# Kernel tuning notes

Hardware: AMD Instinct MI355X
Metric: run time of the kernel (lower is better)

The kernel has to match this reference:

```python
import jax, jax.numpy as jnp
import numpy as np

L = 3        # num_hidden_layers
H = 512      # hidden_features
DIN = 4      # in_features
D = DIN - 1  # u-branch input dim
N = 65536    # batch of query points


def setup_inputs() -> dict:
    key = jax.random.key(0)
    ks = jax.random.split(key, 16)

    def w(k, shape, fan_in):
        # kaiming-normal-ish init (relu), matches init_weights_normal in spirit
        return jax.random.normal(k, shape, jnp.float32) * (2.0 / fan_in) ** 0.5

    return {
        "coords": jax.random.normal(ks[0], (N, DIN), jnp.float32),
        # net_u: (D->H), then (H->H) x (L-1)
        "Wu0": w(ks[1], (D, H), D), "bu0": jnp.zeros((H,), jnp.float32),
        "Wu": w(ks[2], (L - 1, H, H), H), "bu": jnp.zeros((L - 1, H), jnp.float32),
        # net_zu_u: (H->H) x L
        "Wzuu": w(ks[3], (L, H, H), H), "bzuu": jnp.zeros((L, H), jnp.float32),
        # net_z_zu: (H->H) x (L-1), last (H->1), no bias
        "Wzzu": w(ks[4], (L - 1, H, H), H), "Wzzu_last": w(ks[5], (H, 1), H),
        # net_yu_u: (D->1), then (H->1) x L
        "Wyuu0": w(ks[6], (D, 1), D), "byuu0": jnp.zeros((1,), jnp.float32),
        "Wyuu": w(ks[7], (L, H, 1), H), "byuu": jnp.zeros((L, 1), jnp.float32),
        # net_z_yu: (1->H) x L, last (1->1), no bias
        "Wzyu": w(ks[8], (L, 1, H), 1), "Wzyu_last": w(ks[9], (1, 1), 1),
        # net_z_u: (D->H), (H->H) x (L-1), last (H->1)
        "Wzu0": w(ks[10], (D, H), D), "bzu0": jnp.zeros((H,), jnp.float32),
        "Wzu": w(ks[11], (L - 1, H, H), H), "bzu": jnp.zeros((L - 1, H), jnp.float32),
        "Wzu_last": w(ks[12], (H, 1), H), "bzu_last": jnp.zeros((1,), jnp.float32),
        # learned scalar scales
        "p": jnp.float32(0.1), "pu": jnp.float32(0.1), "pzu": jnp.float32(0.1),
    }


def reference(coords, Wu0, bu0, Wu, bu, Wzuu, bzuu, Wzzu, Wzzu_last,
              Wyuu0, byuu0, Wyuu, byuu, Wzyu, Wzyu_last,
              Wzu0, bzu0, Wzu, bzu, Wzu_last, bzu_last, p, pu, pzu):
    relu = jax.nn.relu  # nonlinearity='relu' -> nl == nl_u == relu; dropout inactive (eval)
    y = coords[..., -1:]   # [N, 1]
    u = coords[..., :-1]   # [N, D]
    # layer 0
    z = (u @ Wzu0 + bzu0) + (y * (u @ Wyuu0 + byuu0)) @ Wzyu[0]  # [N, H]
    z = relu(10.0 * p * z)
    u = relu(10.0 * pu * (u @ Wu0 + bu0))  # [N, H]
    for i in range(1, L + 1):
        zz = z * relu(10.0 * pzu * (u @ Wzuu[i - 1] + bzuu[i - 1]))
        t1 = zz @ (Wzzu[i - 1] if i < L else Wzzu_last)
        t2 = (u @ Wzu[i - 1] + bzu[i - 1]) if i < L else (u @ Wzu_last + bzu_last)
        yy = y * (u @ Wyuu[i - 1] + byuu[i - 1])  # [N, 1]
        t3 = yy @ (Wzyu[i] if i < L else Wzyu_last)
        z = t1 + t2 + t3
        if i == L:
            return z  # [N, 1]
        z_out = relu(10.0 * p * z)
        u = relu(10.0 * pu * (u @ Wu[i - 1] + bu[i - 1]))
        z = z_out
    return z
```

## Files before the change

### kernel.cpp

```cpp
#include <hip/hip_runtime.h>
#include <stdint.h>
#include <stddef.h>


typedef float  f32x4 __attribute__((ext_vector_type(4)));
typedef __bf16 bf16x8 __attribute__((ext_vector_type(8)));

__device__ __forceinline__ int act_idx(int row, int k){
  return ((k>>5)<<11) | ((row>>4)<<9) | (((k>>3)&3)<<7) | ((row&15)<<3) | (k&7);
}

__global__ void prep_weights(const float* __restrict__ Wzuu, const float* __restrict__ Wzzu,
                             const float* __restrict__ Wzu,  const float* __restrict__ Wu,
                             __bf16* __restrict__ Wb)
{
  int gid = blockIdx.x * 256 + threadIdx.x;
  int m   = gid >> 16;
  int rem = gid & 65535;
  int k   = rem >> 7;
  int j0  = (rem & 127) << 2;
  const float* src;
  if      (m < 3) src = Wzuu + (size_t)m     * 262144;
  else if (m < 5) src = Wzzu + (size_t)(m-3) * 262144;
  else if (m < 7) src = Wzu  + (size_t)(m-5) * 262144;
  else            src = Wu   + (size_t)(m-7) * 262144;
  const float4 v = *(const float4*)(src + k*512 + j0);
  const int base = m << 18;
  #pragma unroll
  for (int e = 0; e < 4; ++e){
    const int j = j0 + e;
    const float x = (e==0) ? v.x : (e==1) ? v.y : (e==2) ? v.z : v.w;
    const int off = ((k>>5)<<14) | ((j>>4)<<9)
                  | ((((j&15) | (((k>>3)&3)<<4)))<<3) | (k&7);
    Wb[base + off] = (__bf16)x;
  }
}

__device__ __forceinline__ void gemm_acc(const __bf16* __restrict__ a_lds,
                                         const __bf16* __restrict__ wb,
                                         f32x4 acc[4][4],
                                         int wv, int lane)
{
  const __bf16* wp = wb + ((wv<<2)<<9) + (lane<<3);
  bf16x8 a0[4], a1[4], b0[4], b1[4];
  #pragma unroll
  for (int jt = 0; jt < 4; ++jt)
    b0[jt] = *(const bf16x8*)(wp + (jt<<9));
  #pragma unroll
  for (int rt = 0; rt < 4; ++rt)
    a0[rt] = *(const bf16x8*)(a_lds + (rt<<9) + (lane<<3));
  #pragma unroll
  for (int kt = 0; kt < 16; kt += 2){
    #pragma unroll
    for (int jt = 0; jt < 4; ++jt)
      b1[jt] = *(const bf16x8*)(wp + ((kt+1)<<14) + (jt<<9));
    #pragma unroll
    for (int rt = 0; rt < 4; ++rt)
      a1[rt] = *(const bf16x8*)(a_lds + ((kt+1)<<11) + (rt<<9) + (lane<<3));
    #pragma unroll
    for (int jt = 0; jt < 4; ++jt)
      #pragma unroll
      for (int rt = 0; rt < 4; ++rt)
        acc[rt][jt] = __builtin_amdgcn_mfma_f32_16x16x32_bf16(a0[rt], b0[jt], acc[rt][jt], 0, 0, 0);
    if (kt + 2 < 16){
      #pragma unroll
      for (int jt = 0; jt < 4; ++jt)
        b0[jt] = *(const bf16x8*)(wp + ((kt+2)<<14) + (jt<<9));
      #pragma unroll
      for (int rt = 0; rt < 4; ++rt)
        a0[rt] = *(const bf16x8*)(a_lds + ((kt+2)<<11) + (rt<<9) + (lane<<3));
    }
    #pragma unroll
    for (int jt = 0; jt < 4; ++jt)
      #pragma unroll
      for (int rt = 0; rt < 4; ++rt)
        acc[rt][jt] = __builtin_amdgcn_mfma_f32_16x16x32_bf16(a1[rt], b1[jt], acc[rt][jt], 0, 0, 0);
  }
}

__global__ __launch_bounds__(512, 2) void fc_fused(
    const float* __restrict__ coords,
    const __bf16* __restrict__ Wb,
    const float* __restrict__ Wu0,  const float* __restrict__ bu0,
    const float* __restrict__ bu,
    const float* __restrict__ bzuu,
    const float* __restrict__ Wzzu_last,
    const float* __restrict__ Wyuu0, const float* __restrict__ byuu0,
    const float* __restrict__ Wyuu,  const float* __restrict__ byuu,
    const float* __restrict__ Wzyu,  const float* __restrict__ Wzyu_last,
    const float* __restrict__ Wzu0,  const float* __restrict__ bzu0,
    const float* __restrict__ bzu,
    const float* __restrict__ Wzu_last, const float* __restrict__ bzu_last,
    const float* __restrict__ p, const float* __restrict__ pu, const float* __restrict__ pzu,
    float* __restrict__ out)
{
  __shared__ __align__(16) __bf16 u_lds [32768];
  __shared__ __align__(16) __bf16 zz_lds[32768];

  const int tid  = threadIdx.x;
  const int lane = tid & 63;
  const int wv   = tid >> 6;
  const int n0   = blockIdx.x << 6;

  const float P  = 10.f * p[0];
  const float PU = 10.f * pu[0];
  const float PZ = 10.f * pzu[0];

  const float y_l = coords[(size_t)(n0 + lane)*4 + 3];

  for (int s = tid; s < 4096; s += 512){
    const int row = s >> 6;
    const int k0  = (s & 63) << 3;
    const float* c = coords + (size_t)(n0 + row)*4;
    const float c0 = c[0], c1 = c[1], c2 = c[2], yy = c[3];
    const float s0 = c0*Wyuu0[0] + c1*Wyuu0[1] + c2*Wyuu0[2] + byuu0[0];
    bf16x8 pu8, pz8;
    #pragma unroll
    for (int e = 0; e < 8; ++e){
      const int k = k0 + e;
      const float uv = c0*Wu0[k]  + c1*Wu0[512+k]  + c2*Wu0[1024+k]  + bu0[k];
      pu8[e] = (__bf16)fmaxf(PU*uv, 0.f);
      const float zv = c0*Wzu0[k] + c1*Wzu0[512+k] + c2*Wzu0[1024+k] + bzu0[k]
                     + yy*s0*Wzyu[k];
      pz8[e] = (__bf16)fmaxf(P*zv, 0.f);
    }
    *(bf16x8*)(u_lds  + act_idx(row, k0)) = pu8;
    *(bf16x8*)(zz_lds + act_idx(row, k0)) = pz8;
  }
  __syncthreads();

  f32x4 acc[4][4];

  for (int it = 0; it < 3; ++it){
    float s_val = byuu[it];
    {
      const float* wc = Wyuu + it*512;
      for (int kb = 0; kb < 64; ++kb){
        bf16x8 v = *(const bf16x8*)(u_lds + act_idx(lane, kb<<3));
        #pragma unroll
        for (int e = 0; e < 8; ++e) s_val += (float)v[e] * wc[(kb<<3)+e];
      }
    }

    #pragma unroll
    for (int rt = 0; rt < 4; ++rt)
      #pragma unroll
      for (int jt = 0; jt < 4; ++jt)
        acc[rt][jt] = (f32x4){0.f,0.f,0.f,0.f};
    gemm_acc(u_lds, Wb + ((size_t)it<<18), acc, wv, lane);
    #pragma unroll
    for (int jt = 0; jt < 4; ++jt){
      const int col = (wv<<6) + (jt<<4) + (lane & 15);
      const float bz = bzuu[it*512 + col];
      #pragma unroll
      for (int rt = 0; rt < 4; ++rt){
        #pragma unroll
        for (int rr = 0; rr < 4; ++rr){
          const int row = (rt<<4) + ((lane>>4)<<2) + rr;
          const int idx = act_idx(row, col);
          const float zold = (float)zz_lds[idx];
          const float t    = acc[rt][jt][rr] + bz;
          zz_lds[idx] = (__bf16)(zold * fmaxf(PZ*t, 0.f));
        }
      }
    }
    __syncthreads();

    if (it < 2){
      #pragma unroll
      for (int rt = 0; rt < 4; ++rt)
        #pragma unroll
        for (int jt = 0; jt < 4; ++jt)
          acc[rt][jt] = (f32x4){0.f,0.f,0.f,0.f};
      gemm_acc(zz_lds, Wb + ((size_t)(3+it)<<18), acc, wv, lane);
      gemm_acc(u_lds,  Wb + ((size_t)(5+it)<<18), acc, wv, lane);
      __syncthreads();

      float yvv[4][4], svv[4][4];
      #pragma unroll
      for (int rt = 0; rt < 4; ++rt)
        #pragma unroll
        for (int rr = 0; rr < 4; ++rr){
          const int row = (rt<<4) + ((lane>>4)<<2) + rr;
          yvv[rt][rr] = __shfl(y_l,  row);
          svv[rt][rr] = __shfl(s_val, row);
        }
      #pragma unroll
      for (int jt = 0; jt < 4; ++jt){
        const int col = (wv<<6) + (jt<<4) + (lane & 15);
        const float bz  = bzu[it*512 + col];
        const float wzy = Wzyu[(it+1)*512 + col];
        #pragma unroll
        for (int rt = 0; rt < 4; ++rt){
          #pragma unroll
          for (int rr = 0; rr < 4; ++rr){
            const int row = (rt<<4) + ((lane>>4)<<2) + rr;
            const float zn = acc[rt][jt][rr] + bz + yvv[rt][rr]*svv[rt][rr]*wzy;
            zz_lds[act_idx(row, col)] = (__bf16)fmaxf(P*zn, 0.f);
          }
        }
      }

      #pragma unroll
      for (int rt = 0; rt < 4; ++rt)
        #pragma unroll
        for (int jt = 0; jt < 4; ++jt)
          acc[rt][jt] = (f32x4){0.f,0.f,0.f,0.f};
      gemm_acc(u_lds, Wb + ((size_t)(7+it)<<18), acc, wv, lane);
      __syncthreads();
      #pragma unroll
      for (int jt = 0; jt < 4; ++jt){
        const int col = (wv<<6) + (jt<<4) + (lane & 15);
        const float bb = bu[it*512 + col];
        #pragma unroll
        for (int rt = 0; rt < 4; ++rt){
          #pragma unroll
          for (int rr = 0; rr < 4; ++rr){
            const int row = (rt<<4) + ((lane>>4)<<2) + rr;
            u_lds[act_idx(row, col)] = (__bf16)fmaxf(PU*(acc[rt][jt][rr] + bb), 0.f);
          }
        }
      }
      __syncthreads();
    } else {
      const int row = tid >> 3;
      const int q   = tid & 7;
      float av = 0.f, au = 0.f;
      for (int kb = q*8; kb < q*8 + 8; ++kb){
        const int k0 = kb << 3;
        bf16x8 vz = *(const bf16x8*)(zz_lds + act_idx(row, k0));
        bf16x8 vu = *(const bf16x8*)(u_lds  + act_idx(row, k0));
        #pragma unroll
        for (int e = 0; e < 8; ++e){
          av += (float)vz[e] * Wzzu_last[k0+e];
          au += (float)vu[e] * Wzu_last [k0+e];
        }
      }
      float tot = av + au;
      tot += __shfl_xor(tot, 1);
      tot += __shfl_xor(tot, 2);
      tot += __shfl_xor(tot, 4);
      const float yv = __shfl(y_l,  row & 63);
      const float sv = __shfl(s_val, row & 63);
      if (q == 0)
        out[n0 + row] = tot + bzu_last[0] + yv*sv*Wzyu_last[0];
    }
  }
}

extern "C" void kernel_launch(void* const* d_in, const int* in_sizes, int n_in,
                              void* d_out, int out_size, void* d_ws, size_t ws_size,
                              hipStream_t stream)
{
  const float* coords    = (const float*)d_in[0];
  const float* Wu0       = (const float*)d_in[1];
  const float* bu0       = (const float*)d_in[2];
  const float* Wu        = (const float*)d_in[3];
  const float* bu        = (const float*)d_in[4];
  const float* Wzuu      = (const float*)d_in[5];
  const float* bzuu      = (const float*)d_in[6];
  const float* Wzzu      = (const float*)d_in[7];
  const float* Wzzu_last = (const float*)d_in[8];
  const float* Wyuu0     = (const float*)d_in[9];
  const float* byuu0     = (const float*)d_in[10];
  const float* Wyuu      = (const float*)d_in[11];
  const float* byuu      = (const float*)d_in[12];
  const float* Wzyu      = (const float*)d_in[13];
  const float* Wzyu_last = (const float*)d_in[14];
  const float* Wzu0      = (const float*)d_in[15];
  const float* bzu0      = (const float*)d_in[16];
  const float* Wzu       = (const float*)d_in[17];
  const float* bzu       = (const float*)d_in[18];
  const float* Wzu_last  = (const float*)d_in[19];
  const float* bzu_last  = (const float*)d_in[20];
  const float* p         = (const float*)d_in[21];
  const float* pu        = (const float*)d_in[22];
  const float* pzu       = (const float*)d_in[23];

  __bf16* Wb = (__bf16*)d_ws;

  prep_weights<<<2304, 256, 0, stream>>>(Wzuu, Wzzu, Wzu, Wu, Wb);

  fc_fused<<<1024, 512, 0, stream>>>(
      coords, Wb,
      Wu0, bu0, bu, bzuu, Wzzu_last,
      Wyuu0, byuu0, Wyuu, byuu, Wzyu, Wzyu_last,
      Wzu0, bzu0, bzu, Wzu_last, bzu_last,
      p, pu, pzu,
      (float*)d_out);
}
```

Baseline: 408.0 us.

## Prefetch next GEMM weights across calls and split the yu dot product across waves

The GEMM helper now keeps a three-deep ring of weight fragments and, in its last two k-steps, loads the first two weight fragments of the next GEMM in the chain. This is meant to hide global-load latency at GEMM boundaries and through each k-loop. The per-row Wyuu dot product was previously computed redundantly by every wave with 64 serial loads per lane. It is now split across the 8 waves, reduced with shuffles, and combined through a small shared-memory buffer. The extra live fragment registers raise register pressure under launch_bounds(512,2), which could cause spills.

```diff
diff --git a/kernel.cpp b/kernel.cpp
--- a/kernel.cpp
+++ b/kernel.cpp
@@ -38,43 +38,41 @@
 
 __device__ __forceinline__ void gemm_acc(const __bf16* __restrict__ a_lds,
                                          const __bf16* __restrict__ wb,
+                                         const __bf16* __restrict__ wb_next,
+                                         bf16x8 bpre[2][4],
                                          f32x4 acc[4][4],
                                          int wv, int lane)
 {
-  const __bf16* wp = wb + ((wv<<2)<<9) + (lane<<3);
-  bf16x8 a0[4], a1[4], b0[4], b1[4];
+  const int woff = ((wv<<2)<<9) + (lane<<3);
+  const __bf16* wp = wb + woff;
+  bf16x8 b[3][4];
+  bf16x8 a[2][4];
   #pragma unroll
-  for (int jt = 0; jt < 4; ++jt)
-    b0[jt] = *(const bf16x8*)(wp + (jt<<9));
+  for (int jt = 0; jt < 4; ++jt){ b[0][jt] = bpre[0][jt]; b[1][jt] = bpre[1][jt]; }
   #pragma unroll
   for (int rt = 0; rt < 4; ++rt)
-    a0[rt] = *(const bf16x8*)(a_lds + (rt<<9) + (lane<<3));
+    a[0][rt] = *(const bf16x8*)(a_lds + (rt<<9) + (lane<<3));
   #pragma unroll
-  for (int kt = 0; kt < 16; kt += 2){
+  for (int kt = 0; kt < 16; ++kt){
+    if (kt < 14){
+      #pragma unroll
+      for (int jt = 0; jt < 4; ++jt)
+        b[(kt+2)%3][jt] = *(const bf16x8*)(wp + ((kt+2)<<14) + (jt<<9));
+    } else {
+      #pragma unroll
+      for (int jt = 0; jt < 4; ++jt)
+        bpre[kt-14][jt] = *(const bf16x8*)(wb_next + woff + ((kt-14)<<14) + (jt<<9));
+    }
+    if (kt < 15){
+      #pragma unroll
+      for (int rt = 0; rt < 4; ++rt)
+        a[(kt+1)&1][rt] = *(const bf16x8*)(a_lds + ((kt+1)<<11) + (rt<<9) + (lane<<3));
+    }
     #pragma unroll
     for (int jt = 0; jt < 4; ++jt)
-      b1[jt] = *(const bf16x8*)(wp + ((kt+1)<<14) + (jt<<9));
-    #pragma unroll
-    for (int rt = 0; rt < 4; ++rt)
-      a1[rt] = *(const bf16x8*)(a_lds + ((kt+1)<<11) + (rt<<9) + (lane<<3));
-    #pragma unroll
-    for (int jt = 0; jt < 4; ++jt)
-      #pragma unroll
-      for (int rt = 0; rt < 4; ++rt)
-        acc[rt][jt] = __builtin_amdgcn_mfma_f32_16x16x32_bf16(a0[rt], b0[jt], acc[rt][jt], 0, 0, 0);
-    if (kt + 2 < 16){
-      #pragma unroll
-      for (int jt = 0; jt < 4; ++jt)
-        b0[jt] = *(const bf16x8*)(wp + ((kt+2)<<14) + (jt<<9));
-      #pragma unroll
-      for (int rt = 0; rt < 4; ++rt)
-        a0[rt] = *(const bf16x8*)(a_lds + ((kt+2)<<11) + (rt<<9) + (lane<<3));
-    }
-    #pragma unroll
-    for (int jt = 0; jt < 4; ++jt)
-      #pragma unroll
-      for (int rt = 0; rt < 4; ++rt)
-        acc[rt][jt] = __builtin_amdgcn_mfma_f32_16x16x32_bf16(a1[rt], b1[jt], acc[rt][jt], 0, 0, 0);
+      #pragma unroll
+      for (int rt = 0; rt < 4; ++rt)
+        acc[rt][jt] = __builtin_amdgcn_mfma_f32_16x16x32_bf16(a[kt&1][rt], b[kt%3][jt], acc[rt][jt], 0, 0, 0);
   }
 }
 
@@ -96,6 +94,7 @@
 {
   __shared__ __align__(16) __bf16 u_lds [32768];
   __shared__ __align__(16) __bf16 zz_lds[32768];
+  __shared__ float sp_lds[2][64];
 
   const int tid  = threadIdx.x;
   const int lane = tid & 63;
@@ -107,6 +106,16 @@
   const float PZ = 10.f * pzu[0];
 
   const float y_l = coords[(size_t)(n0 + lane)*4 + 3];
+
+  bf16x8 bpre[2][4];
+  {
+    const int woff = ((wv<<2)<<9) + (lane<<3);
+    #pragma unroll
+    for (int s2 = 0; s2 < 2; ++s2)
+      #pragma unroll
+      for (int jt = 0; jt < 4; ++jt)
+        bpre[s2][jt] = *(const bf16x8*)(Wb + woff + (s2<<14) + (jt<<9));
+  }
 
   for (int s = tid; s < 4096; s += 512){
     const int row = s >> 6;
@@ -132,14 +141,31 @@
   f32x4 acc[4][4];
 
   for (int it = 0; it < 3; ++it){
-    float s_val = byuu[it];
+    const __bf16* w_p1 = Wb + ((size_t)it     << 18);
+    const __bf16* w_zz = Wb + ((size_t)(3+it) << 18);
+    const __bf16* w_zu = Wb + ((size_t)(5+it) << 18);
+    const __bf16* w_u  = Wb + ((size_t)(7+it) << 18);
+    const __bf16* w_n1 = (it < 2) ? w_zz : w_p1;
+    const __bf16* w_nx = (it < 2) ? (Wb + ((size_t)(it+1) << 18)) : w_p1;
+
     {
-      const float* wc = Wyuu + it*512;
-      for (int kb = 0; kb < 64; ++kb){
-        bf16x8 v = *(const bf16x8*)(u_lds + act_idx(lane, kb<<3));
-        #pragma unroll
-        for (int e = 0; e < 8; ++e) s_val += (float)v[e] * wc[(kb<<3)+e];
-      }
+      const float* wc = Wyuu + (it<<9);
+      const int rt = wv & 3;
+      const int kh = wv >> 2;
+      float pp = 0.f;
+      #pragma unroll
+      for (int t = 0; t < 8; ++t){
+        const int kt = (kh<<3) + t;
+        const int k0 = (kt<<5) + ((lane>>4)<<3);
+        bf16x8 v = *(const bf16x8*)(u_lds + (kt<<11) + (rt<<9) + (lane<<3));
+        const float4 w0 = *(const float4*)(wc + k0);
+        const float4 w1 = *(const float4*)(wc + k0 + 4);
+        pp += (float)v[0]*w0.x + (float)v[1]*w0.y + (float)v[2]*w0.z + (float)v[3]*w0.w
+            + (float)v[4]*w1.x + (float)v[5]*w1.y + (float)v[6]*w1.z + (float)v[7]*w1.w;
+      }
+      pp += __shfl_xor(pp, 16);
+      pp += __shfl_xor(pp, 32);
+      if (lane < 16) sp_lds[kh][(rt<<4) + lane] = pp;
     }
 
     #pragma unroll
@@ -147,11 +173,11 @@
       #pragma unroll
       for (int jt = 0; jt < 4; ++jt)
         acc[rt][jt] = (f32x4){0.f,0.f,0.f,0.f};
-    gemm_acc(u_lds, Wb + ((size_t)it<<18), acc, wv, lane);
+    gemm_acc(u_lds, w_p1, w_n1, bpre, acc, wv, lane);
     #pragma unroll
     for (int jt = 0; jt < 4; ++jt){
       const int col = (wv<<6) + (jt<<4) + (lane & 15);
-      const float bz = bzuu[it*512 + col];
+      const float bz = bzuu[(it<<9) + col];
       #pragma unroll
       for (int rt = 0; rt < 4; ++rt){
         #pragma unroll
@@ -172,30 +198,30 @@
         #pragma unroll
         for (int jt = 0; jt < 4; ++jt)
           acc[rt][jt] = (f32x4){0.f,0.f,0.f,0.f};
-      gemm_acc(zz_lds, Wb + ((size_t)(3+it)<<18), acc, wv, lane);
-      gemm_acc(u_lds,  Wb + ((size_t)(5+it)<<18), acc, wv, lane);
+      gemm_acc(zz_lds, w_zz, w_zu, bpre, acc, wv, lane);
+      gemm_acc(u_lds,  w_zu, w_u,  bpre, acc, wv, lane);
       __syncthreads();
 
-      float yvv[4][4], svv[4][4];
+      const float by_it = byuu[it];
+      float ysr[4][4];
       #pragma unroll
       for (int rt = 0; rt < 4; ++rt)
         #pragma unroll
         for (int rr = 0; rr < 4; ++rr){
           const int row = (rt<<4) + ((lane>>4)<<2) + rr;
-          yvv[rt][rr] = __shfl(y_l,  row);
-          svv[rt][rr] = __shfl(s_val, row);
+          ysr[rt][rr] = __shfl(y_l, row) * (sp_lds[0][row] + sp_lds[1][row] + by_it);
         }
       #pragma unroll
       for (int jt = 0; jt < 4; ++jt){
         const int col = (wv<<6) + (jt<<4) + (lane & 15);
-        const float bz  = bzu[it*512 + col];
-        const float wzy = Wzyu[(it+1)*512 + col];
+        const float bz  = bzu[(it<<9) + col];
+        const float wzy = Wzyu[((it+1)<<9) + col];
         #pragma unroll
         for (int rt = 0; rt < 4; ++rt){
           #pragma unroll
           for (int rr = 0; rr < 4; ++rr){
             const int row = (rt<<4) + ((lane>>4)<<2) + rr;
-            const float zn = acc[rt][jt][rr] + bz + yvv[rt][rr]*svv[rt][rr]*wzy;
+            const float zn = acc[rt][jt][rr] + bz + ysr[rt][rr]*wzy;
             zz_lds[act_idx(row, col)] = (__bf16)fmaxf(P*zn, 0.f);
           }
         }
@@ -206,12 +232,12 @@
         #pragma unroll
         for (int jt = 0; jt < 4; ++jt)
           acc[rt][jt] = (f32x4){0.f,0.f,0.f,0.f};
-      gemm_acc(u_lds, Wb + ((size_t)(7+it)<<18), acc, wv, lane);
+      gemm_acc(u_lds, w_u, w_nx, bpre, acc, wv, lane);
       __syncthreads();
       #pragma unroll
       for (int jt = 0; jt < 4; ++jt){
         const int col = (wv<<6) + (jt<<4) + (lane & 15);
-        const float bb = bu[it*512 + col];
+        const float bb = bu[(it<<9) + col];
         #pragma unroll
         for (int rt = 0; rt < 4; ++rt){
           #pragma unroll
@@ -240,8 +266,8 @@
       tot += __shfl_xor(tot, 1);
       tot += __shfl_xor(tot, 2);
       tot += __shfl_xor(tot, 4);
-      const float yv = __shfl(y_l,  row & 63);
-      const float sv = __shfl(s_val, row & 63);
+      const float sv = sp_lds[0][row] + sp_lds[1][row] + byuu[2];
+      const float yv = __shfl(y_l, row & 63);
       if (q == 0)
         out[n0 + row] = tot + bzu_last[0] + yv*sv*Wzyu_last[0];
     }
```

Result: slower. 422.1 us (+3.4%).
